# Kernel optimization log

Measured on AMD Instinct MI355X. Metric: run time of the kernel, lower is better.

Reference implementation:

```python
import jax, jax.numpy as jnp
import numpy as np

C, G, S, L, B = 16, 8192, 8, 3, 32


def setup_inputs() -> dict:
    key = jax.random.key(0)
    kx, kI = jax.random.split(key)
    # x: valuation vector over G ground atoms per batch element, in [0,1)
    x = jax.random.uniform(kx, (B, G), dtype=jnp.float32)
    # I: precomputed index tensor [C, G, S, L], indices into the G axis of x
    I = jax.random.randint(kI, (C, G, S, L), 0, G, dtype=jnp.int64)
    return {"x": x, "I": I}


def reference(x, I):
    # Equivalent of: for each clause i, gather(V_tild, 1, I_i) -> prod over L -> sum over S
    # torch gather semantics: out[b, g, s, l] = x[b, I[i, g, s, l]]
    # Vectorized over all clauses at once; no repeat/broadcast materialization beyond the gather.
    gathered = x[:, I]                        # [B, C, G, S, L]
    body = jnp.prod(gathered, axis=-1)        # conjunction over L body literals -> [B, C, G, S]
    clause_val = jnp.sum(body, axis=-1)       # sum over S substitutions -> [B, C, G]
    # torch.stack over clauses puts C first: [C, B, G]
    return jnp.transpose(clause_val, (1, 0, 2))
```

## Files before the change

kernel.cpp:

```cpp
#include <hip/hip_runtime.h>

#define Cc 16
#define Gg 8192
#define Ss 8
#define Ll 3
#define Bb 32

#define SLICES 16
#define THREADS 512

__device__ __forceinline__ void async_load16(const void* gsrc, void* lds) {
    uint32_t l32 = (uint32_t)__builtin_amdgcn_readfirstlane((uint32_t)(uintptr_t)lds);
    __builtin_amdgcn_global_load_lds(
        (const __attribute__((address_space(1))) uint32_t*)(uintptr_t)gsrc,
        (__attribute__((address_space(3))) uint32_t*)(uintptr_t)l32,
        16, 0, 0);
}

__device__ __forceinline__ void stage_slice(const float2* gsrc, float2* ldst, int tid) {
    const char* g = (const char*)gsrc;
    char* l = (char*)ldst;
    const int lane = tid & 63;
    const int w = tid >> 6;
    #pragma unroll
    for (int i = 0; i < 8; ++i) {
        int off = ((i << 3) | w) << 10;
        async_load16(g + off + lane * 16, l + off);
    }
}

__global__ __launch_bounds__(256) void build_xpairs(const float* __restrict__ x,
                                                    float2* __restrict__ xs) {
    int t = blockIdx.x * 256 + threadIdx.x;
    int z = t >> 13;
    int g = t & (Gg - 1);
    float a = x[(size_t)(2 * z) * Gg + g];
    float b = x[(size_t)(2 * z + 1) * Gg + g];
    xs[t] = make_float2(a, b);
}

__global__ __launch_bounds__(THREADS) void clause_all(const float2* __restrict__ xs,
                                                      const int* __restrict__ I,
                                                      float* __restrict__ out) {
    __shared__ float2 buf[2 * Gg];
    const int tid = threadIdx.x;
    const int flat = blockIdx.x * THREADS + tid;
    const int c = flat >> 13;
    const int g = flat & (Gg - 1);

    stage_slice(xs, buf, tid);

    const int4* I4 = (const int4*)(I + ((size_t)c * Gg + g) * (Ss * Ll));
    int4 q0 = I4[0], q1 = I4[1], q2 = I4[2], q3 = I4[3], q4 = I4[4], q5 = I4[5];
    int idx[Ss * Ll] = {q0.x, q0.y, q0.z, q0.w, q1.x, q1.y, q1.z, q1.w,
                        q2.x, q2.y, q2.z, q2.w, q3.x, q3.y, q3.z, q3.w,
                        q4.x, q4.y, q4.z, q4.w, q5.x, q5.y, q5.z, q5.w};

    float* op = out + ((size_t)(c * Bb)) * Gg + g;

    #pragma unroll 1
    for (int z = 0; z < SLICES; ++z) {
        __syncthreads();
        float2* cur = buf + (z & 1) * Gg;
        if (z + 1 < SLICES)
            stage_slice(xs + (size_t)(z + 1) * Gg, buf + ((z + 1) & 1) * Gg, tid);

        float2 v[Ss * Ll];
        #pragma unroll
        for (int k = 0; k < Ss * Ll; ++k)
            v[k] = cur[idx[k]];

        float2 s = {0.f, 0.f};
        #pragma unroll
        for (int q = 0; q < Ss; ++q) {
            s.x += v[3 * q].x * v[3 * q + 1].x * v[3 * q + 2].x;
            s.y += v[3 * q].y * v[3 * q + 1].y * v[3 * q + 2].y;
        }

        op[(size_t)(2 * z) * Gg] = s.x;
        op[(size_t)(2 * z + 1) * Gg] = s.y;
    }
}

__global__ __launch_bounds__(256) void clause_kernel_direct(const float* __restrict__ x,
                                                            const int* __restrict__ I,
                                                            float* __restrict__ out) {
    const int tid = threadIdx.x;
    const int b = tid & 31;
    const int j = tid >> 5;
    const int g = blockIdx.x * 8 + j;
    const int c = blockIdx.y;

    const int* Icg = I + (size_t)(c * Gg + g) * (Ss * Ll);
    float sum = 0.f;
    #pragma unroll
    for (int s = 0; s < Ss; ++s) {
        float p0 = x[(size_t)b * Gg + Icg[3 * s + 0]];
        float p1 = x[(size_t)b * Gg + Icg[3 * s + 1]];
        float p2 = x[(size_t)b * Gg + Icg[3 * s + 2]];
        sum += p0 * p1 * p2;
    }
    out[(size_t)(c * Bb + b) * Gg + g] = sum;
}

extern "C" void kernel_launch(void* const* d_in, const int* in_sizes, int n_in,
                              void* d_out, int out_size, void* d_ws, size_t ws_size,
                              hipStream_t stream) {
    const float* x = (const float*)d_in[0];
    const int* I = (const int*)d_in[1];
    float* out = (float*)d_out;

    const size_t xs_bytes = (size_t)SLICES * Gg * sizeof(float2);

    if (ws_size >= xs_bytes) {
        float2* xs = (float2*)d_ws;
        build_xpairs<<<(SLICES * Gg) / 256, 256, 0, stream>>>(x, xs);
        clause_all<<<(Cc * Gg) / THREADS, THREADS, 0, stream>>>(xs, I, out);
    } else {
        clause_kernel_direct<<<dim3(Gg / 8, Cc), 256, 0, stream>>>(x, I, out);
    }
}
```

Before: 91.52 us.

## Gather bf16-packed x with 16-bit indices, splitting batch across grid

Measured after the change: 89.77 us. Within noise of the previous version (-1.9%).

```diff
diff --git a/kernel.cpp b/kernel.cpp
--- a/kernel.cpp
+++ b/kernel.cpp
@@ -1,4 +1,5 @@
 #include <hip/hip_runtime.h>
+#include <stdint.h>
 
 #define Cc 16
 #define Gg 8192
@@ -6,7 +7,7 @@
 #define Ll 3
 #define Bb 32
 
-#define SLICES 16
+#define ZS 4
 #define THREADS 512
 
 __device__ __forceinline__ void async_load16(const void* gsrc, void* lds) {
@@ -17,69 +18,94 @@
         16, 0, 0);
 }
 
-__device__ __forceinline__ void stage_slice(const float2* gsrc, float2* ldst, int tid) {
-    const char* g = (const char*)gsrc;
-    char* l = (char*)ldst;
-    const int lane = tid & 63;
-    const int w = tid >> 6;
-    #pragma unroll
-    for (int i = 0; i < 8; ++i) {
-        int off = ((i << 3) | w) << 10;
-        async_load16(g + off + lane * 16, l + off);
-    }
+__device__ __forceinline__ uint32_t f2bf(float f) {
+    uint32_t u = __float_as_uint(f);
+    return (u + 0x7fffu + ((u >> 16) & 1u)) >> 16;
 }
 
-__global__ __launch_bounds__(256) void build_xpairs(const float* __restrict__ x,
-                                                    float2* __restrict__ xs) {
+__global__ __launch_bounds__(256) void pack_idx(const int* __restrict__ I,
+                                                ushort* __restrict__ I16) {
+    int t = blockIdx.x * 256 + threadIdx.x;
+    int4 v = ((const int4*)I)[t];
+    ushort4 o = { (ushort)v.x, (ushort)v.y, (ushort)v.z, (ushort)v.w };
+    ((ushort4*)I16)[t] = o;
+}
+
+__global__ __launch_bounds__(256) void build_xh(const float* __restrict__ x,
+                                                uint4* __restrict__ xh) {
     int t = blockIdx.x * 256 + threadIdx.x;
     int z = t >> 13;
     int g = t & (Gg - 1);
-    float a = x[(size_t)(2 * z) * Gg + g];
-    float b = x[(size_t)(2 * z + 1) * Gg + g];
-    xs[t] = make_float2(a, b);
+    uint32_t w[4];
+    #pragma unroll
+    for (int j = 0; j < 4; ++j) {
+        uint32_t lo = f2bf(x[(size_t)(8 * z + 2 * j) * Gg + g]);
+        uint32_t hi = f2bf(x[(size_t)(8 * z + 2 * j + 1) * Gg + g]);
+        w[j] = lo | (hi << 16);
+    }
+    xh[t] = make_uint4(w[0], w[1], w[2], w[3]);
 }
 
-__global__ __launch_bounds__(THREADS) void clause_all(const float2* __restrict__ xs,
-                                                      const int* __restrict__ I,
-                                                      float* __restrict__ out) {
-    __shared__ float2 buf[2 * Gg];
+__global__ __launch_bounds__(THREADS) void clause_bf16(const uint4* __restrict__ xh,
+                                                       const ushort* __restrict__ I16,
+                                                       float* __restrict__ out) {
+    __shared__ uint4 xl[Gg];
     const int tid = threadIdx.x;
+    const int z = blockIdx.y;
     const int flat = blockIdx.x * THREADS + tid;
     const int c = flat >> 13;
     const int g = flat & (Gg - 1);
 
-    stage_slice(xs, buf, tid);
+    {
+        const char* gs = (const char*)(xh + (size_t)z * Gg);
+        char* ls = (char*)xl;
+        const int lane = tid & 63;
+        const int w = tid >> 6;
+        #pragma unroll
+        for (int i = 0; i < 16; ++i) {
+            int off = ((w << 4) | i) << 10;
+            async_load16(gs + off + lane * 16, ls + off);
+        }
+    }
 
-    const int4* I4 = (const int4*)(I + ((size_t)c * Gg + g) * (Ss * Ll));
-    int4 q0 = I4[0], q1 = I4[1], q2 = I4[2], q3 = I4[3], q4 = I4[4], q5 = I4[5];
-    int idx[Ss * Ll] = {q0.x, q0.y, q0.z, q0.w, q1.x, q1.y, q1.z, q1.w,
-                        q2.x, q2.y, q2.z, q2.w, q3.x, q3.y, q3.z, q3.w,
-                        q4.x, q4.y, q4.z, q4.w, q5.x, q5.y, q5.z, q5.w};
+    const uint4* ip = (const uint4*)(I16 + (size_t)(c * Gg + g) * (Ss * Ll));
+    uint4 i0 = ip[0], i1 = ip[1], i2 = ip[2];
 
-    float* op = out + ((size_t)(c * Bb)) * Gg + g;
+    __syncthreads();
 
-    #pragma unroll 1
-    for (int z = 0; z < SLICES; ++z) {
-        __syncthreads();
-        float2* cur = buf + (z & 1) * Gg;
-        if (z + 1 < SLICES)
-            stage_slice(xs + (size_t)(z + 1) * Gg, buf + ((z + 1) & 1) * Gg, tid);
+    uint32_t wd[12] = {i0.x, i0.y, i0.z, i0.w, i1.x, i1.y, i1.z, i1.w,
+                       i2.x, i2.y, i2.z, i2.w};
+    uint4 v[Ss * Ll];
+    #pragma unroll
+    for (int k = 0; k < Ss * Ll; ++k) {
+        uint32_t idx = (k & 1) ? (wd[k >> 1] >> 16) : (wd[k >> 1] & 0xffffu);
+        v[k] = xl[idx];
+    }
 
-        float2 v[Ss * Ll];
+    float acc[8] = {0.f, 0.f, 0.f, 0.f, 0.f, 0.f, 0.f, 0.f};
+    #pragma unroll
+    for (int s = 0; s < Ss; ++s) {
+        const uint4 a = v[3 * s], b = v[3 * s + 1], d = v[3 * s + 2];
+        const uint32_t* ua = &a.x;
+        const uint32_t* ub = &b.x;
+        const uint32_t* ud = &d.x;
         #pragma unroll
-        for (int k = 0; k < Ss * Ll; ++k)
-            v[k] = cur[idx[k]];
+        for (int j = 0; j < 4; ++j) {
+            float a0 = __uint_as_float(ua[j] << 16);
+            float a1 = __uint_as_float(ua[j] & 0xffff0000u);
+            float b0 = __uint_as_float(ub[j] << 16);
+            float b1 = __uint_as_float(ub[j] & 0xffff0000u);
+            float d0 = __uint_as_float(ud[j] << 16);
+            float d1 = __uint_as_float(ud[j] & 0xffff0000u);
+            acc[2 * j]     += a0 * b0 * d0;
+            acc[2 * j + 1] += a1 * b1 * d1;
+        }
+    }
 
-        float2 s = {0.f, 0.f};
-        #pragma unroll
-        for (int q = 0; q < Ss; ++q) {
-            s.x += v[3 * q].x * v[3 * q + 1].x * v[3 * q + 2].x;
-            s.y += v[3 * q].y * v[3 * q + 1].y * v[3 * q + 2].y;
-        }
-
-        op[(size_t)(2 * z) * Gg] = s.x;
-        op[(size_t)(2 * z + 1) * Gg] = s.y;
-    }
+    float* op = out + ((size_t)(c * Bb + z * 8)) * Gg + g;
+    #pragma unroll
+    for (int j = 0; j < 8; ++j)
+        op[(size_t)j * Gg] = acc[j];
 }
 
 __global__ __launch_bounds__(256) void clause_kernel_direct(const float* __restrict__ x,
@@ -110,12 +136,16 @@
     const int* I = (const int*)d_in[1];
     float* out = (float*)d_out;
 
-    const size_t xs_bytes = (size_t)SLICES * Gg * sizeof(float2);
+    const size_t nIdx = (size_t)Cc * Gg * Ss * Ll;
+    const size_t xh_bytes = (size_t)ZS * Gg * sizeof(uint4);
+    const size_t i16_bytes = nIdx * sizeof(ushort);
 
-    if (ws_size >= xs_bytes) {
-        float2* xs = (float2*)d_ws;
-        build_xpairs<<<(SLICES * Gg) / 256, 256, 0, stream>>>(x, xs);
-        clause_all<<<(Cc * Gg) / THREADS, THREADS, 0, stream>>>(xs, I, out);
+    if (ws_size >= xh_bytes + i16_bytes) {
+        uint4* xh = (uint4*)d_ws;
+        ushort* I16 = (ushort*)((char*)d_ws + xh_bytes);
+        pack_idx<<<(int)(nIdx / 4 / 256), 256, 0, stream>>>(I, I16);
+        build_xh<<<(ZS * Gg) / 256, 256, 0, stream>>>(x, xh);
+        clause_bf16<<<dim3((Cc * Gg) / THREADS, ZS), THREADS, 0, stream>>>(xh, I16, out);
     } else {
         clause_kernel_direct<<<dim3(Gg / 8, Cc), 256, 0, stream>>>(x, I, out);
     }
```
